# Kernel tuning notes

Measured on AMD Instinct MI355X. Metric: run time of the kernel, lower is better.

The kernel has to match this reference:

```python
import math
import jax, jax.numpy as jnp
import numpy as np

SR = 48000.0
HARMONIC_NUM = 8
SINE_AMP = 0.1
NOISE_STD = 0.003


def setup_inputs() -> dict:
    key = jax.random.key(0)
    k1, k2, k3 = jax.random.split(key, 3)
    B, T = 16, 400
    H = HARMONIC_NUM
    # F0 contour in Hz, uniform [0, 400)
    f0 = jax.random.uniform(k1, (B, T), dtype=jnp.float32) * 400.0
    # tiny merge linear: (harmonic_num+1) -> 1
    W = jax.random.normal(k2, (1, H + 1), dtype=jnp.float32) * (1.0 / math.sqrt(H + 1))
    b = jax.random.normal(k3, (1,), dtype=jnp.float32) * 0.01
    return {"f0": f0, "upp": 512, "W": W, "b": b}


def reference(f0, upp, W, b):
    # f0: (B, T) Hz -> nearest-neighbor upsample by integer factor upp: (B, Tu, 1)
    f0_up = jnp.repeat(f0, upp, axis=1)[..., None]
    rad = f0_up / SR  # normalized freq per sample, (B, Tu, 1)
    # multipliers 1..H+1: fundamental + harmonics 2..H+1 (torch uses rad*(k+1), k=1..H)
    m = jnp.arange(1, HARMONIC_NUM + 2, dtype=f0.dtype)  # (H+1,)
    phase = jnp.cumsum(rad * m, axis=1) * jnp.asarray(2.0 * math.pi, f0.dtype)
    sine_waves = jnp.sin(phase) * SINE_AMP  # (B, Tu, H+1)
    uv = (f0_up > 1.0).astype(f0.dtype)  # (B, Tu, 1)
    noise_amp = uv * NOISE_STD + (1.0 - uv) * (SINE_AMP / 3.0)
    noise = noise_amp * jax.random.normal(jax.random.key(42), sine_waves.shape, sine_waves.dtype)
    src = sine_waves * uv + noise  # (B, Tu, H+1)
    out = jnp.tanh(src @ W.T + b)  # (B, Tu, 1)
    return jnp.transpose(out, (0, 2, 1))  # (B, 1, Tu)
```

## Files before the change

### kernel.cpp

```cpp
#include <hip/hip_runtime.h>
#include <math.h>
#include <stdint.h>

#define NB 16
#define NT 400
#define UPP 512
#define TUP (NT * UPP)
#define NH 9
#define NSAMP (NB * TUP)

__device__ __forceinline__ uint32_t rotl32(uint32_t x, uint32_t d) {
  return (x << d) | (x >> (32u - d));
}

__device__ __forceinline__ void tf2x32(uint32_t& x0, uint32_t& x1) {
  const uint32_t ks0 = 0u;
  const uint32_t ks1 = 42u;
  const uint32_t ks2 = 0x1BD11BDAu ^ 0u ^ 42u;
  x0 += ks0; x1 += ks1;
#define TFR(r) { x0 += x1; x1 = rotl32(x1, r); x1 ^= x0; }
  TFR(13) TFR(15) TFR(26) TFR(6)
  x0 += ks1; x1 += ks2 + 1u;
  TFR(17) TFR(29) TFR(16) TFR(24)
  x0 += ks2; x1 += ks0 + 2u;
  TFR(13) TFR(15) TFR(26) TFR(6)
  x0 += ks0; x1 += ks1 + 3u;
  TFR(17) TFR(29) TFR(16) TFR(24)
  x0 += ks1; x1 += ks2 + 4u;
  TFR(13) TFR(15) TFR(26) TFR(6)
  x0 += ks2; x1 += ks0 + 5u;
#undef TFR
}

#if defined(__has_builtin)
#if __has_builtin(__builtin_amdgcn_sinf)
#define HW_SIN_REV(x) __builtin_amdgcn_sinf(x)
#endif
#if __has_builtin(__builtin_amdgcn_cosf)
#define HW_COS_REV(x) __builtin_amdgcn_cosf(x)
#endif
#if __has_builtin(__builtin_amdgcn_fractf)
#define FRACT_F32(x) __builtin_amdgcn_fractf(x)
#endif
#if __has_builtin(__builtin_amdgcn_logf)
#define HW_LOG2(x) __builtin_amdgcn_logf(x)
#endif
#if __has_builtin(__builtin_amdgcn_sqrtf)
#define HW_SQRT(x) __builtin_amdgcn_sqrtf(x)
#endif
#endif
#ifndef HW_SIN_REV
#define HW_SIN_REV(x) __sinf(6.283185307179586f * (x))
#endif
#ifndef HW_COS_REV
#define HW_COS_REV(x) __cosf(6.283185307179586f * (x))
#endif
#ifndef FRACT_F32
#define FRACT_F32(x) ((x) - floorf(x))
#endif
#ifndef HW_LOG2
#define HW_LOG2(x) __log2f(x)
#endif
#ifndef HW_SQRT
#define HW_SQRT(x) __fsqrt_rn(x)
#endif

__device__ __forceinline__ float bits_to_pu(uint32_t bits) {
  float f = __uint_as_float((bits >> 9) | 0x3f800000u) - 1.0f;
  const float lo = -0.99999994f;
  float u = fmaf(f, 2.0f, lo);
  u = fmaxf(u, lo);
  float x2 = (1.0f - u) * (1.0f + u);
  float L = HW_LOG2(x2);
  float w = fmaf(-0.69314718f, L, -2.5f);
  float p = 2.81022636e-08f;
  p = fmaf(p, w, 3.43273939e-07f);
  p = fmaf(p, w, -3.5233877e-06f);
  p = fmaf(p, w, -4.39150654e-06f);
  p = fmaf(p, w, 0.00021858087f);
  p = fmaf(p, w, -0.00125372503f);
  p = fmaf(p, w, -0.00417768164f);
  p = fmaf(p, w, 0.246640727f);
  p = fmaf(p, w, 1.50140941f);
  bool tail = L <= -7.2134752f;
  if (__builtin_expect(__any(tail), 0)) {
    if (tail) {
      float t = HW_SQRT(-0.69314718f * L) - 3.0f;
      float q = -0.000200214257f;
      q = fmaf(q, t, 0.000100950558f);
      q = fmaf(q, t, 0.00134934322f);
      q = fmaf(q, t, -0.00367342844f);
      q = fmaf(q, t, 0.00573950773f);
      q = fmaf(q, t, -0.0076224613f);
      q = fmaf(q, t, 0.00943887047f);
      q = fmaf(q, t, 1.00167406f);
      q = fmaf(q, t, 2.83297682f);
      p = q;
    }
  }
  return p * u;
}

__global__ __launch_bounds__(512) void snsf_main(const float* __restrict__ f0,
                                                 const float* __restrict__ W,
                                                 const float* __restrict__ bptr,
                                                 float* __restrict__ out) {
  __shared__ double spart[8];

  int fb = blockIdx.x;
  int bb = fb / NT;
  int j  = fb - bb * NT;
  int r  = threadIdx.x;
  int s  = bb * TUP + (j << 9) + r;

  const float* row = f0 + bb * NT;
  double v = (r < j) ? (double)row[r] : 0.0;
#pragma unroll
  for (int off = 32; off >= 1; off >>= 1) v += __shfl_xor(v, off);
  if ((r & 63) == 0) spart[r >> 6] = v;
  __syncthreads();
  double sum = spart[0] + spart[1] + spart[2] + spart[3] +
               spart[4] + spart[5] + spart[6] + spart[7];
  double tphase = sum * (512.0 / 48000.0);
  float B0v = (float)(tphase - floor(tphase));

  float f0v = row[j];
  float rad = f0v * (1.0f / 48000.0f);
  bool uv = f0v > 1.0f;
  float ampP = uv ? 0.0042426409f : 0.047140453f;
  float samp = uv ? 0.1f : 0.0f;

  float theta = fmaf((float)(r + 1), rad, B0v);
  float fr = FRACT_F32(theta);
  float z_cur = HW_SIN_REV(fr);
  float c = HW_COS_REV(fr);
  float c2 = c + c;
  float z_prev = 0.0f;

  float pre = bptr[0];
  uint32_t base9 = 9u * (uint32_t)s;
#pragma unroll
  for (int h = 0; h < NH; ++h) {
    uint32_t x0 = 0u;
    uint32_t x1 = base9 + (uint32_t)h;
    tf2x32(x0, x1);
    float pu = bits_to_pu(x0 ^ x1);

    float srcv = fmaf(samp, z_cur, ampP * pu);
    pre = fmaf(W[h], srcv, pre);

    float z_next = fmaf(c2, z_cur, -z_prev);
    z_prev = z_cur;
    z_cur = z_next;
  }

  float x2 = pre * pre;
  out[s] = pre * fmaf(x2, fmaf(x2, 0.13333334f, -0.33333334f), 1.0f);
}

extern "C" void kernel_launch(void* const* d_in, const int* in_sizes, int n_in,
                              void* d_out, int out_size, void* d_ws, size_t ws_size,
                              hipStream_t stream) {
  const float* f0 = (const float*)d_in[0];
  const float* W = (const float*)d_in[2];
  const float* b = (const float*)d_in[3];
  float* out = (float*)d_out;

  snsf_main<<<dim3(NB * NT), dim3(512), 0, stream>>>(f0, W, b, out);
}
```

Measured before the change: 121.7 us.

## Process multiple samples per thread and split batches across three kernel variants

```diff
diff --git a/kernel.cpp b/kernel.cpp
--- a/kernel.cpp
+++ b/kernel.cpp
@@ -13,23 +13,31 @@
   return (x << d) | (x >> (32u - d));
 }
 
-__device__ __forceinline__ void tf2x32(uint32_t& x0, uint32_t& x1) {
-  const uint32_t ks0 = 0u;
+template <int N>
+__device__ __forceinline__ void tf2x32_multi(uint32_t* x0, uint32_t* x1) {
   const uint32_t ks1 = 42u;
   const uint32_t ks2 = 0x1BD11BDAu ^ 0u ^ 42u;
-  x0 += ks0; x1 += ks1;
-#define TFR(r) { x0 += x1; x1 = rotl32(x1, r); x1 ^= x0; }
-  TFR(13) TFR(15) TFR(26) TFR(6)
-  x0 += ks1; x1 += ks2 + 1u;
-  TFR(17) TFR(29) TFR(16) TFR(24)
-  x0 += ks2; x1 += ks0 + 2u;
-  TFR(13) TFR(15) TFR(26) TFR(6)
-  x0 += ks0; x1 += ks1 + 3u;
-  TFR(17) TFR(29) TFR(16) TFR(24)
-  x0 += ks1; x1 += ks2 + 4u;
-  TFR(13) TFR(15) TFR(26) TFR(6)
-  x0 += ks2; x1 += ks0 + 5u;
-#undef TFR
+#define TFRN(r)                                                      \
+  _Pragma("unroll") for (int i = 0; i < N; ++i) {                    \
+    x0[i] += x1[i]; x1[i] = rotl32(x1[i], r); x1[i] ^= x0[i];        \
+  }
+#define INJN(a, b)                                                   \
+  _Pragma("unroll") for (int i = 0; i < N; ++i) {                    \
+    x0[i] += (a); x1[i] += (b);                                      \
+  }
+  INJN(0u, ks1)
+  TFRN(13) TFRN(15) TFRN(26) TFRN(6)
+  INJN(ks1, ks2 + 1u)
+  TFRN(17) TFRN(29) TFRN(16) TFRN(24)
+  INJN(ks2, 0u + 2u)
+  TFRN(13) TFRN(15) TFRN(26) TFRN(6)
+  INJN(0u, ks1 + 3u)
+  TFRN(17) TFRN(29) TFRN(16) TFRN(24)
+  INJN(ks1, ks2 + 4u)
+  TFRN(13) TFRN(15) TFRN(26) TFRN(6)
+  INJN(ks2, 0u + 5u)
+#undef TFRN
+#undef INJN
 }
 
 #if defined(__has_builtin)
@@ -65,13 +73,14 @@
 #define HW_SQRT(x) __fsqrt_rn(x)
 #endif
 
-__device__ __forceinline__ float bits_to_pu(uint32_t bits) {
+__device__ __forceinline__ float pu_main(uint32_t bits, float& L, float& u) {
   float f = __uint_as_float((bits >> 9) | 0x3f800000u) - 1.0f;
   const float lo = -0.99999994f;
-  float u = fmaf(f, 2.0f, lo);
-  u = fmaxf(u, lo);
-  float x2 = (1.0f - u) * (1.0f + u);
-  float L = HW_LOG2(x2);
+  float uu = fmaf(f, 2.0f, lo);
+  uu = fmaxf(uu, lo);
+  u = uu;
+  float x2 = (1.0f - uu) * (1.0f + uu);
+  L = HW_LOG2(x2);
   float w = fmaf(-0.69314718f, L, -2.5f);
   float p = 2.81022636e-08f;
   p = fmaf(p, w, 3.43273939e-07f);
@@ -82,45 +91,50 @@
   p = fmaf(p, w, -0.00417768164f);
   p = fmaf(p, w, 0.246640727f);
   p = fmaf(p, w, 1.50140941f);
-  bool tail = L <= -7.2134752f;
-  if (__builtin_expect(__any(tail), 0)) {
-    if (tail) {
-      float t = HW_SQRT(-0.69314718f * L) - 3.0f;
-      float q = -0.000200214257f;
-      q = fmaf(q, t, 0.000100950558f);
-      q = fmaf(q, t, 0.00134934322f);
-      q = fmaf(q, t, -0.00367342844f);
-      q = fmaf(q, t, 0.00573950773f);
-      q = fmaf(q, t, -0.0076224613f);
-      q = fmaf(q, t, 0.00943887047f);
-      q = fmaf(q, t, 1.00167406f);
-      q = fmaf(q, t, 2.83297682f);
-      p = q;
-    }
-  }
-  return p * u;
-}
-
-__global__ __launch_bounds__(512) void snsf_main(const float* __restrict__ f0,
-                                                 const float* __restrict__ W,
-                                                 const float* __restrict__ bptr,
-                                                 float* __restrict__ out) {
-  __shared__ double spart[8];
+  return p;
+}
+
+__device__ __forceinline__ float pu_tail(float L) {
+  float t = HW_SQRT(-0.69314718f * L) - 3.0f;
+  float q = -0.000200214257f;
+  q = fmaf(q, t, 0.000100950558f);
+  q = fmaf(q, t, 0.00134934322f);
+  q = fmaf(q, t, -0.00367342844f);
+  q = fmaf(q, t, 0.00573950773f);
+  q = fmaf(q, t, -0.0076224613f);
+  q = fmaf(q, t, 0.00943887047f);
+  q = fmaf(q, t, 1.00167406f);
+  q = fmaf(q, t, 2.83297682f);
+  return q;
+}
+
+template <int SPT>
+__global__ __launch_bounds__(UPP / SPT) void snsf_kern(
+    const float* __restrict__ f0, const float* __restrict__ W,
+    const float* __restrict__ bptr, float* __restrict__ out, int bb_base) {
+  constexpr int THREADS = UPP / SPT;
+  constexpr int NWAVE = THREADS / 64;
+  __shared__ double spart[NWAVE];
 
   int fb = blockIdx.x;
-  int bb = fb / NT;
-  int j  = fb - bb * NT;
+  int bb = bb_base + fb / NT;
+  int j  = fb - (fb / NT) * NT;
   int r  = threadIdx.x;
-  int s  = bb * TUP + (j << 9) + r;
 
   const float* row = f0 + bb * NT;
-  double v = (r < j) ? (double)row[r] : 0.0;
+  double v = 0.0;
+#pragma unroll
+  for (int k = 0; k < (NT + THREADS - 1) / THREADS; ++k) {
+    int idx = r + k * THREADS;
+    if (idx < j) v += (double)row[idx];
+  }
 #pragma unroll
   for (int off = 32; off >= 1; off >>= 1) v += __shfl_xor(v, off);
   if ((r & 63) == 0) spart[r >> 6] = v;
   __syncthreads();
-  double sum = spart[0] + spart[1] + spart[2] + spart[3] +
-               spart[4] + spart[5] + spart[6] + spart[7];
+  double sum = 0.0;
+#pragma unroll
+  for (int wv = 0; wv < NWAVE; ++wv) sum += spart[wv];
   double tphase = sum * (512.0 / 48000.0);
   float B0v = (float)(tphase - floor(tphase));
 
@@ -130,32 +144,71 @@
   float ampP = uv ? 0.0042426409f : 0.047140453f;
   float samp = uv ? 0.1f : 0.0f;
 
-  float theta = fmaf((float)(r + 1), rad, B0v);
-  float fr = FRACT_F32(theta);
-  float z_cur = HW_SIN_REV(fr);
-  float c = HW_COS_REV(fr);
-  float c2 = c + c;
-  float z_prev = 0.0f;
-
-  float pre = bptr[0];
-  uint32_t base9 = 9u * (uint32_t)s;
+  int t0 = SPT * r;
+  int s0 = bb * TUP + (j << 9) + t0;
+
+  float z[SPT], zp[SPT], c2[SPT], pre[SPT];
+#pragma unroll
+  for (int i = 0; i < SPT; ++i) {
+    float th = fmaf((float)(t0 + i + 1), rad, B0v);
+    float fr = FRACT_F32(th);
+    z[i] = HW_SIN_REV(fr);
+    float c = HW_COS_REV(fr);
+    c2[i] = c + c;
+    zp[i] = 0.0f;
+    pre[i] = bptr[0];
+  }
+
+  uint32_t base9 = 9u * (uint32_t)s0;
 #pragma unroll
   for (int h = 0; h < NH; ++h) {
-    uint32_t x0 = 0u;
-    uint32_t x1 = base9 + (uint32_t)h;
-    tf2x32(x0, x1);
-    float pu = bits_to_pu(x0 ^ x1);
-
-    float srcv = fmaf(samp, z_cur, ampP * pu);
-    pre = fmaf(W[h], srcv, pre);
-
-    float z_next = fmaf(c2, z_cur, -z_prev);
-    z_prev = z_cur;
-    z_cur = z_next;
-  }
-
-  float x2 = pre * pre;
-  out[s] = pre * fmaf(x2, fmaf(x2, 0.13333334f, -0.33333334f), 1.0f);
+    uint32_t x0[SPT], x1[SPT];
+#pragma unroll
+    for (int i = 0; i < SPT; ++i) {
+      x0[i] = 0u;
+      x1[i] = base9 + (uint32_t)(9 * i + h);
+    }
+    tf2x32_multi<SPT>(x0, x1);
+    float L[SPT], u[SPT], p[SPT];
+    bool anytail = false;
+#pragma unroll
+    for (int i = 0; i < SPT; ++i) {
+      p[i] = pu_main(x0[i] ^ x1[i], L[i], u[i]);
+      anytail = anytail || (L[i] <= -7.2134752f);
+    }
+    if (__builtin_expect(__any(anytail), 0)) {
+#pragma unroll
+      for (int i = 0; i < SPT; ++i)
+        if (L[i] <= -7.2134752f) p[i] = pu_tail(L[i]);
+    }
+#pragma unroll
+    for (int i = 0; i < SPT; ++i) {
+      float pu = p[i] * u[i];
+      float srcv = fmaf(samp, z[i], ampP * pu);
+      pre[i] = fmaf(W[h], srcv, pre[i]);
+      float zn = fmaf(c2[i], z[i], -zp[i]);
+      zp[i] = z[i];
+      z[i] = zn;
+    }
+  }
+
+  float o[SPT];
+#pragma unroll
+  for (int i = 0; i < SPT; ++i) {
+    float x2v = pre[i] * pre[i];
+    o[i] = pre[i] * fmaf(x2v, fmaf(x2v, 0.13333334f, -0.33333334f), 1.0f);
+  }
+  if constexpr (SPT == 2) {
+    *reinterpret_cast<float2*>(out + s0) = make_float2(o[0], o[1]);
+  } else if constexpr (SPT == 4) {
+    *reinterpret_cast<float4*>(out + s0) = make_float4(o[0], o[1], o[2], o[3]);
+  } else if constexpr (SPT == 8) {
+    *reinterpret_cast<float4*>(out + s0) = make_float4(o[0], o[1], o[2], o[3]);
+    *reinterpret_cast<float4*>(out + s0 + 4) = make_float4(o[4], o[5], o[6], o[7]);
+  } else {
+#pragma unroll
+    for (int i = 0; i < SPT; ++i) out[s0 + i] = o[i];
+  }
 }
 
 extern "C" void kernel_launch(void* const* d_in, const int* in_sizes, int n_in,
@@ -166,5 +219,7 @@
   const float* b = (const float*)d_in[3];
   float* out = (float*)d_out;
 
-  snsf_main<<<dim3(NB * NT), dim3(512), 0, stream>>>(f0, W, b, out);
-}
+  snsf_kern<2><<<dim3(4 * NT), dim3(256), 0, stream>>>(f0, W, b, out, 0);
+  snsf_kern<4><<<dim3(6 * NT), dim3(128), 0, stream>>>(f0, W, b, out, 4);
+  snsf_kern<8><<<dim3(6 * NT), dim3(64), 0, stream>>>(f0, W, b, out, 10);
+}
```

Result: slower. 143.3 us (+17.8%).
